# Kernel tuning notes

Hardware: AMD Instinct MI355X
Metric: run time of the kernel (lower is better)

## Reference

```python
import jax, jax.numpy as jnp
import numpy as np

EPS = 1e-12

def _spectral_normalize(W, u):
    # torch spectral_norm (eval-time math): v = normalize(W^T u), sigma = u^T W v
    u = jax.lax.stop_gradient(u)
    v = W.T @ u
    v = jax.lax.stop_gradient(v / (jnp.linalg.norm(v) + EPS))
    sigma = u @ (W @ v)
    return W / sigma

def _conv1x1(x, W):
    # 1x1 conv, no bias: (out,in) x (B,in,H,W) -> (B,out,H,W)
    return jnp.einsum('oc,bchw->bohw', W, x)

def setup_inputs() -> dict:
    key = jax.random.key(0)
    ks = jax.random.split(key, 10)
    B, C, H, W = 4, 512, 64, 64
    Cp = C // 8
    return {
        'x': jax.random.normal(ks[0], (B, C, H, W), jnp.float32),
        'Wf': jax.random.normal(ks[1], (Cp, C), jnp.float32) * 0.05,
        'Wg': jax.random.normal(ks[2], (Cp, C), jnp.float32) * 0.05,
        'Wh': jax.random.normal(ks[3], (Cp, C), jnp.float32) * 0.05,
        'Wv': jax.random.normal(ks[4], (C, Cp), jnp.float32) * 0.05,
        'uf': jax.random.normal(ks[5], (Cp,), jnp.float32),
        'ug': jax.random.normal(ks[6], (Cp,), jnp.float32),
        'uh': jax.random.normal(ks[7], (Cp,), jnp.float32),
        'uv': jax.random.normal(ks[8], (C,), jnp.float32),
        'gamma': jax.random.normal(ks[9], (1,), jnp.float32) * 0.1,
    }

def reference(x, Wf, Wg, Wh, Wv, uf, ug, uh, uv, gamma):
    B, C, H, W = x.shape
    Cp = Wf.shape[0]
    N = H * W
    Wf_sn = _spectral_normalize(Wf, uf)
    Wg_sn = _spectral_normalize(Wg, ug)
    Wh_sn = _spectral_normalize(Wh, uh)
    Wv_sn = _spectral_normalize(Wv, uv)
    fx = _conv1x1(x, Wf_sn).reshape(B, Cp, N)   # (B,Cp,N)
    gx = _conv1x1(x, Wg_sn).reshape(B, Cp, N)   # (B,Cp,N)
    # fx^T gx: (B,N,N), unscaled single-head attention, softmax over last dim
    scores = jnp.einsum('bcn,bcm->bnm', fx, gx)
    attn = jax.nn.softmax(scores, axis=-1)
    hx = _conv1x1(x, Wh_sn).reshape(B, Cp, N)
    # hx @ attn: out[b,c,j] = sum_i hx[b,c,i] * attn[b,i,j]
    out = jnp.einsum('bci,bij->bcj', hx, attn).reshape(B, Cp, H, W)
    unscaled = _conv1x1(out, Wv_sn)
    return gamma * unscaled + x
```

## Files before the change

### kernel.cpp

```cpp
#include <hip/hip_runtime.h>


#define NB 4
#define CC 512
#define CP 64
#define NN 4096
#define L2E 1.4426950408889634f

typedef __attribute__((ext_vector_type(8))) short short8;
typedef __attribute__((ext_vector_type(4))) float floatx4;
typedef __attribute__((ext_vector_type(16))) float floatx16;

#define MFMA32(A, B, C) __builtin_amdgcn_mfma_f32_32x32x16_bf16((A), (B), (C), 0, 0, 0)

__device__ __forceinline__ float bf2f_u(unsigned short h) {
    return __uint_as_float((unsigned)h << 16);
}
__device__ __forceinline__ float bf16lo(unsigned v) { return __uint_as_float(v << 16); }
__device__ __forceinline__ float bf16hi(unsigned v) { return __uint_as_float(v & 0xffff0000u); }
__device__ __forceinline__ unsigned short f2bf(float f) {
    unsigned u = __float_as_uint(f);
    u += 0x7fffu + ((u >> 16) & 1u);
    return (unsigned short)(u >> 16);
}
__device__ __forceinline__ unsigned pack2bf(float a, float b) {
    return (unsigned)f2bf(a) | ((unsigned)f2bf(b) << 16);
}
__device__ __forceinline__ float ldS(const void* p, long i, int f32) {
    return f32 ? ((const float*)p)[i] : bf2f_u(((const unsigned short*)p)[i]);
}
__device__ __forceinline__ float4 ld4(const void* p, long i, int f32) {
    if (f32) return *reinterpret_cast<const float4*>((const float*)p + i);
    uint2 v = *reinterpret_cast<const uint2*>((const unsigned short*)p + i);
    return make_float4(bf16lo(v.x), bf16hi(v.x), bf16lo(v.y), bf16hi(v.y));
}
__device__ __forceinline__ short8 frag8(const void* p, long i, int f32) {
    uint4 au;
    if (f32) {
        float4 v0 = *reinterpret_cast<const float4*>((const float*)p + i);
        float4 v1 = *reinterpret_cast<const float4*>((const float*)p + i + 4);
        au.x = pack2bf(v0.x, v0.y); au.y = pack2bf(v0.z, v0.w);
        au.z = pack2bf(v1.x, v1.y); au.w = pack2bf(v1.z, v1.w);
    } else {
        au = *reinterpret_cast<const uint4*>((const unsigned short*)p + i);
    }
    return *reinterpret_cast<short8*>(&au);
}
__device__ __forceinline__ short8 as_s8(uint4 v) { return *reinterpret_cast<short8*>(&v); }
__device__ __forceinline__ floatx16 zero16() {
    floatx16 z;
    #pragma unroll
    for (int i = 0; i < 16; ++i) z[i] = 0.f;
    return z;
}
__device__ __forceinline__ unsigned cvtpk_bf16(float a, float b) {
    unsigned r;
    asm("v_cvt_pk_bf16_f32 %0, %1, %2" : "=v"(r) : "v"(a), "v"(b));
    return r;
}
__device__ __forceinline__ void pl32swap(unsigned &a, unsigned &b) {
    asm("v_permlane32_swap_b32 %0, %1" : "+v"(a), "+v"(b));
}
__device__ __forceinline__ float rcpf(float x) {
    float r;
    asm("v_rcp_f32 %0, %1" : "=v"(r) : "v"(x));
    return r;
}
__device__ __forceinline__ float exp2a(float x) {
    float r;
    asm("v_exp_f32 %0, %1" : "=v"(r) : "v"(x));
    return r;
}

__global__ __launch_bounds__(256) void detect_kernel(
    const unsigned* __restrict__ x, int* __restrict__ flag)
{
    __shared__ int red[256];
    const int t = threadIdx.x;
    int bad = 0;
    for (int i = t; i < 4096; i += 256) {
        unsigned w = x[i];
        float f0 = __uint_as_float(w << 16);
        float f1 = __uint_as_float(w & 0xffff0000u);
        float a0 = fabsf(f0), a1 = fabsf(f1);
        if (!(a0 <= 1e3f) || (f0 != 0.f && a0 < 1e-20f)) bad++;
        if (!(a1 <= 1e3f) || (f1 != 0.f && a1 < 1e-20f)) bad++;
    }
    red[t] = bad;
    __syncthreads();
    for (int s = 128; s > 0; s >>= 1) { if (t < s) red[t] += red[t + s]; __syncthreads(); }
    if (t == 0) *flag = (red[0] > 64) ? 1 : 0;
}

__global__ __launch_bounds__(256) void xpose_kernel(
    const void* __restrict__ x, const int* __restrict__ dflag,
    unsigned short* __restrict__ xTF)
{
    const int f32 = *dflag;
    const int nt = blockIdx.x;
    const int b  = blockIdx.y;
    const int n0 = nt * 32;
    const int t = threadIdx.x;
    __shared__ unsigned short xl[32][72];

    const int n_l = t & 31, cg8 = ((t >> 5) & 7) * 8;
    const int q = t >> 6, lo = t & 63;

    for (int slab = 0; slab < 8; ++slab) {
        const int cs = slab * 64;
        float v[8];
        #pragma unroll
        for (int j = 0; j < 8; ++j)
            v[j] = ldS(x, ((long)b * CC + cs + cg8 + j) * NN + n0 + n_l, f32);
        if (slab) __syncthreads();
        unsigned* row = reinterpret_cast<unsigned*>(&xl[n_l][cg8]);
        row[0] = pack2bf(v[0], v[1]);
        row[1] = pack2bf(v[2], v[3]);
        row[2] = pack2bf(v[4], v[5]);
        row[3] = pack2bf(v[6], v[7]);
        __syncthreads();
        const int cb = q * 16 + ((lo >> 5) << 3);
        uint4 val = *reinterpret_cast<const uint4*>(&xl[lo & 31][cb]);
        size_t off = (((size_t)(b * 128 + nt) * 32) + slab * 4 + q) * 512 + (size_t)lo * 8;
        *reinterpret_cast<uint4*>(xTF + off) = val;
    }
}

__global__ __launch_bounds__(512) void sigma_kernel(
    const void* __restrict__ Wf, const void* __restrict__ Wg,
    const void* __restrict__ Wh, const void* __restrict__ Wv,
    const void* __restrict__ uf, const void* __restrict__ ug,
    const void* __restrict__ uh, const void* __restrict__ uv,
    const int* __restrict__ dflag, float* __restrict__ sig)
{
    const int f32 = *dflag;
    const int w = blockIdx.x;
    const void* W;
    const void* u;
    if (w == 0)      { W = Wf; u = uf; }
    else if (w == 1) { W = Wg; u = ug; }
    else if (w == 2) { W = Wh; u = uh; }
    else             { W = Wv; u = uv; }

    __shared__ float us[512];
    __shared__ float red[512];
    const int t = threadIdx.x;
    float S;

    if (w < 3) {
        if (t < 64) us[t] = ldS(u, t, f32);
        __syncthreads();
        float a = 0.f;
        #pragma unroll
        for (int i = 0; i < 64; ++i)
            a = fmaf(ldS(W, (long)i * 512 + t, f32), us[i], a);
        red[t] = a * a;
        __syncthreads();
        #pragma unroll
        for (int s = 256; s > 0; s >>= 1) {
            if (t < s) red[t] += red[t + s];
            __syncthreads();
        }
        S = red[0];
    } else {
        us[t] = ldS(u, t, f32);
        __syncthreads();
        const int g = t >> 6, c = t & 63;
        float a = 0.f;
        #pragma unroll
        for (int k = 0; k < 64; ++k) {
            int i = g + k * 8;
            a = fmaf(ldS(W, (long)i * 64 + c, f32), us[i], a);
        }
        red[t] = a;
        __syncthreads();
        #pragma unroll
        for (int s = 256; s >= 64; s >>= 1) {
            if (t < s) red[t] += red[t + s];
            __syncthreads();
        }
        float ac = (t < 64) ? red[t] : 0.f;
        __syncthreads();
        red[t] = ac * ac;
        __syncthreads();
        #pragma unroll
        for (int s = 256; s > 0; s >>= 1) {
            if (t < s) red[t] += red[t + s];
            __syncthreads();
        }
        S = red[0];
    }
    if (t == 0) sig[w] = (sqrtf(S) + 1e-12f) / S;
}

__global__ __launch_bounds__(256) void wprep_kernel(
    const void* __restrict__ Wf, const void* __restrict__ Wg,
    const void* __restrict__ Wh,
    const int* __restrict__ dflag, const float* __restrict__ sig,
    unsigned short* __restrict__ WF)
{
    const int f32 = *dflag;
    const int idx = blockIdx.x * 256 + threadIdx.x;
    const int l   = idx & 63;
    const int kc  = (idx >> 6) & 31;
    const int cpt = (idx >> 11) & 1;
    const int wi  = idx >> 12;
    const void* W = (wi == 0) ? Wf : ((wi == 1) ? Wg : Wh);
    const float sc = sig[wi] * (wi == 0 ? L2E : 1.f);
    const int cp = cpt * 32 + (l & 31);
    const int c  = kc * 16 + ((l >> 5) << 3);
    const long base = (long)cp * CC + c;
    float a0 = ldS(W, base + 0, f32) * sc, a1 = ldS(W, base + 1, f32) * sc;
    float a2 = ldS(W, base + 2, f32) * sc, a3 = ldS(W, base + 3, f32) * sc;
    float a4 = ldS(W, base + 4, f32) * sc, a5 = ldS(W, base + 5, f32) * sc;
    float a6 = ldS(W, base + 6, f32) * sc, a7 = ldS(W, base + 7, f32) * sc;
    uint4 o;
    o.x = pack2bf(a0, a1); o.y = pack2bf(a2, a3);
    o.z = pack2bf(a4, a5); o.w = pack2bf(a6, a7);
    *reinterpret_cast<uint4*>(WF + (size_t)idx * 8) = o;
}

__global__ __launch_bounds__(256, 4) void proj_kernel(
    const unsigned short* __restrict__ xTF,
    const unsigned short* __restrict__ WF,
    unsigned short* __restrict__ fxF, unsigned short* __restrict__ gxF,
    unsigned short* __restrict__ hxF)
{
    const int t = threadIdx.x;
    const int w = t >> 6, l = t & 63;
    const int b  = blockIdx.y;
    const int zc = blockIdx.z;
    const int wi = zc >> 1, cpt = zc & 1;
    const int nt = blockIdx.x * 4 + w;

    const unsigned short* xb = xTF + ((size_t)(b * 128 + nt) * 32) * 512 + (size_t)l * 8;
    const unsigned short* wb = WF + ((size_t)zc * 32) * 512 + (size_t)l * 8;

    floatx16 accE = zero16(), accO = zero16();
    uint4 x0 = *reinterpret_cast<const uint4*>(xb);
    uint4 w0 = *reinterpret_cast<const uint4*>(wb);
    uint4 x1, w1;

    if (wi == 2) {
        for (int kc = 0; kc < 32; kc += 2) {
            x1 = *reinterpret_cast<const uint4*>(xb + (kc + 1) * 512);
            w1 = *reinterpret_cast<const uint4*>(wb + (kc + 1) * 512);
            accE = MFMA32(as_s8(x0), as_s8(w0), accE);
            if (kc + 2 < 32) {
                x0 = *reinterpret_cast<const uint4*>(xb + (kc + 2) * 512);
                w0 = *reinterpret_cast<const uint4*>(wb + (kc + 2) * 512);
            }
            accO = MFMA32(as_s8(x1), as_s8(w1), accO);
        }
    } else {
        for (int kc = 0; kc < 32; kc += 2) {
            x1 = *reinterpret_cast<const uint4*>(xb + (kc + 1) * 512);
            w1 = *reinterpret_cast<const uint4*>(wb + (kc + 1) * 512);
            accE = MFMA32(as_s8(w0), as_s8(x0), accE);
            if (kc + 2 < 32) {
                x0 = *reinterpret_cast<const uint4*>(xb + (kc + 2) * 512);
                w0 = *reinterpret_cast<const uint4*>(wb + (kc + 2) * 512);
            }
            accO = MFMA32(as_s8(w1), as_s8(x1), accO);
        }
    }

    float a[16];
    #pragma unroll
    for (int i = 0; i < 16; ++i) a[i] = accE[i] + accO[i];

    if (wi < 2) {
        unsigned short* __restrict__ dstF = (wi == 0) ? fxF : gxF;
        #pragma unroll
        for (int kcl = 0; kcl < 2; ++kcl) {
            const int r8 = kcl * 8;
            unsigned u0 = cvtpk_bf16(a[r8 + 0], a[r8 + 1]);
            unsigned u1 = cvtpk_bf16(a[r8 + 2], a[r8 + 3]);
            unsigned u2 = cvtpk_bf16(a[r8 + 4], a[r8 + 5]);
            unsigned u3 = cvtpk_bf16(a[r8 + 6], a[r8 + 7]);
            pl32swap(u0, u2);
            pl32swap(u1, u3);
            uint4 o = make_uint4(u0, u1, u2, u3);
            size_t off = (((size_t)(b * 128 + nt) * 4) + cpt * 2 + kcl) * 512 + (size_t)l * 8;
            *reinterpret_cast<uint4*>(dstF + off) = o;
        }
    } else {
        #pragma unroll
        for (int ich = 0; ich < 2; ++ich) {
            const int r8 = ich * 8;
            unsigned u0 = cvtpk_bf16(a[r8 + 0], a[r8 + 1]);
            unsigned u1 = cvtpk_bf16(a[r8 + 2], a[r8 + 3]);
            unsigned u2 = cvtpk_bf16(a[r8 + 4], a[r8 + 5]);
            unsigned u3 = cvtpk_bf16(a[r8 + 6], a[r8 + 7]);
            pl32swap(u0, u2);
            pl32swap(u1, u3);
            uint4 o = make_uint4(u0, u1, u2, u3);
            size_t off = ((((size_t)(b * 128 + nt) * 2 + ich) * 2) + cpt) * 512 + (size_t)l * 8;
            *reinterpret_cast<uint4*>(hxF + off) = o;
        }
    }
}

__global__ __launch_bounds__(256, 4) void rowstats_kernel(
    const unsigned short* __restrict__ fxF, const unsigned short* __restrict__ gxF,
    float* __restrict__ rl)
{
    const int t = threadIdx.x;
    const int w = t >> 6, l = t & 63, l31 = l & 31, hi = l >> 5;
    const int b = blockIdx.z;
    const int i0 = blockIdx.x * 128 + w * 32;
    const int jbase = blockIdx.y * (NN / 8);

    __shared__ unsigned short stg[2][2048];

    const unsigned short* fA = fxF + ((size_t)(b * 128 + (i0 >> 5))) * 2048 + (size_t)l * 8;
    uint4 af[4];
    #pragma unroll
    for (int kc = 0; kc < 4; ++kc)
        af[kc] = *reinterpret_cast<const uint4*>(fA + kc * 512);

    const unsigned short* gB = gxF + ((size_t)(b * 128 + (jbase >> 5))) * 2048
                               + (size_t)w * 512 + (size_t)l * 8;

    float suml[16];
    #pragma unroll
    for (int r = 0; r < 16; ++r) suml[r] = 0.f;

    uint4 rg = *reinterpret_cast<const uint4*>(gB);
    *reinterpret_cast<uint4*>(&stg[0][w * 512 + l * 8]) = rg;
    __syncthreads();

    #pragma unroll 2
    for (int jt = 0; jt < 16; ++jt) {
        const int cur = jt & 1;
        if (jt + 1 < 16)
            rg = *reinterpret_cast<const uint4*>(gB + (size_t)(jt + 1) * 2048);

        uint4 bf[4];
        #pragma unroll
        for (int kc = 0; kc < 4; ++kc)
            bf[kc] = *reinterpret_cast<const uint4*>(&stg[cur][kc * 512 + l * 8]);

        floatx16 s = zero16();
        #pragma unroll
        for (int kc = 0; kc < 4; ++kc)
            s = MFMA32(as_s8(af[kc]), as_s8(bf[kc]), s);
        #pragma unroll
        for (int r = 0; r < 16; ++r) suml[r] += exp2a(s[r]);

        if (jt + 1 < 16)
            *reinterpret_cast<uint4*>(&stg[cur ^ 1][w * 512 + l * 8]) = rg;
        __syncthreads();
    }

    #pragma unroll
    for (int r = 0; r < 16; ++r) {
        float v = suml[r];
        v += __shfl_xor(v, 1);
        v += __shfl_xor(v, 2);
        v += __shfl_xor(v, 4);
        v += __shfl_xor(v, 8);
        v += __shfl_xor(v, 16);
        suml[r] = v;
    }
    if (l31 == 0) {
        #pragma unroll
        for (int r = 0; r < 16; ++r) {
            int row = (r & 3) + 8 * (r >> 2) + 4 * hi;
            atomicAdd(&rl[(size_t)b * NN + i0 + row], suml[r]);
        }
    }
}

__global__ __launch_bounds__(256) void scalehx_kernel(
    const float* __restrict__ rl, unsigned short* __restrict__ hxF)
{
    const int idx = blockIdx.x * 256 + threadIdx.x;
    const int l = idx & 63;
    const int r = idx >> 6;
    const int ich = (r >> 1) & 1;
    const int tile = (r >> 2) & 127;
    const int b = r >> 9;
    const int i0 = tile * 32 + ich * 16 + (l >> 5) * 8;
    const float* rp = rl + (size_t)b * NN + i0;
    float4 ra = *reinterpret_cast<const float4*>(rp);
    float4 rb = *reinterpret_cast<const float4*>(rp + 4);
    uint4 v = *reinterpret_cast<uint4*>(hxF + (size_t)idx * 8);
    uint4 ov;
    ov.x = pack2bf(bf16lo(v.x) * rcpf(ra.x), bf16hi(v.x) * rcpf(ra.y));
    ov.y = pack2bf(bf16lo(v.y) * rcpf(ra.z), bf16hi(v.y) * rcpf(ra.w));
    ov.z = pack2bf(bf16lo(v.z) * rcpf(rb.x), bf16hi(v.z) * rcpf(rb.y));
    ov.w = pack2bf(bf16lo(v.w) * rcpf(rb.z), bf16hi(v.w) * rcpf(rb.w));
    *reinterpret_cast<uint4*>(hxF + (size_t)idx * 8) = ov;
}

__global__ __launch_bounds__(256, 4) void pv_kernel(
    const unsigned short* __restrict__ fxF, const unsigned short* __restrict__ gxF,
    const unsigned short* __restrict__ hxF,
    float* __restrict__ opF0, float* __restrict__ opF1,
    float* __restrict__ opF2, float* __restrict__ opF3)
{
    const int t = threadIdx.x;
    const int w = t >> 6, l = t & 63, l31 = l & 31, hi = l >> 5;
    const int igrp = w >> 1, jgrp = w & 1;
    const int b = blockIdx.z;
    const int j0 = blockIdx.x * 64;
    const int isb = blockIdx.y;
    const int tbase = isb * 32 + igrp * 16;

    __shared__ unsigned short stg[2][2][2][2048];
    float* red = reinterpret_cast<float*>(stg);

    uint4 qf[4];
    {
        const unsigned short* gq =
            gxF + ((size_t)(b * 128 + (j0 >> 5) + jgrp)) * 2048 + (size_t)l * 8;
        #pragma unroll
        for (int kc = 0; kc < 4; ++kc)
            qf[kc] = *reinterpret_cast<const uint4*>(gq + kc * 512);
    }

    floatx16 acc0 = zero16(), acc1 = zero16();

    const unsigned short* sb =
        (jgrp == 0 ? fxF : hxF) + ((size_t)(b * 128 + tbase)) * 2048 + (size_t)l * 8;

    uint4 rg0 = *reinterpret_cast<const uint4*>(sb);
    uint4 rg1 = *reinterpret_cast<const uint4*>(sb + 512);
    uint4 rg2 = *reinterpret_cast<const uint4*>(sb + 1024);
    uint4 rg3 = *reinterpret_cast<const uint4*>(sb + 1536);
    {
        unsigned short* d = &stg[igrp][0][jgrp][l * 8];
        *reinterpret_cast<uint4*>(d)        = rg0;
        *reinterpret_cast<uint4*>(d + 512)  = rg1;
        *reinterpret_cast<uint4*>(d + 1024) = rg2;
        *reinterpret_cast<uint4*>(d + 1536) = rg3;
    }
    __syncthreads();

    #pragma unroll 2
    for (int it = 0; it < 16; ++it) {
        const int cur = it & 1;
        if (it + 1 < 16) {
            const unsigned short* p = sb + (size_t)(it + 1) * 2048;
            rg0 = *reinterpret_cast<const uint4*>(p);
            rg1 = *reinterpret_cast<const uint4*>(p + 512);
            rg2 = *reinterpret_cast<const uint4*>(p + 1024);
            rg3 = *reinterpret_cast<const uint4*>(p + 1536);
        }

        const unsigned short* fl = &stg[igrp][cur][0][l * 8];
        const unsigned short* vl = &stg[igrp][cur][1][l * 8];
        uint4 af[4], vf[4];
        #pragma unroll
        for (int kc = 0; kc < 4; ++kc)
            af[kc] = *reinterpret_cast<const uint4*>(fl + kc * 512);
        vf[0] = *reinterpret_cast<const uint4*>(vl);
        vf[1] = *reinterpret_cast<const uint4*>(vl + 1024);
        vf[2] = *reinterpret_cast<const uint4*>(vl + 512);
        vf[3] = *reinterpret_cast<const uint4*>(vl + 1536);

        floatx16 s = zero16();
        #pragma unroll
        for (int kc = 0; kc < 4; ++kc)
            s = MFMA32(as_s8(af[kc]), as_s8(qf[kc]), s);

        float e[16];
        #pragma unroll
        for (int r = 0; r < 16; ++r) e[r] = exp2a(s[r]);

        unsigned u0 = cvtpk_bf16(e[0], e[1]);
        unsigned u1 = cvtpk_bf16(e[2], e[3]);
        unsigned u2 = cvtpk_bf16(e[4], e[5]);
        unsigned u3 = cvtpk_bf16(e[6], e[7]);
        pl32swap(u0, u2);
        pl32swap(u1, u3);
        uint4 pa0 = make_uint4(u0, u1, u2, u3);
        unsigned u4 = cvtpk_bf16(e[8], e[9]);
        unsigned u5 = cvtpk_bf16(e[10], e[11]);
        unsigned u6 = cvtpk_bf16(e[12], e[13]);
        unsigned u7 = cvtpk_bf16(e[14], e[15]);
        pl32swap(u4, u6);
        pl32swap(u5, u7);
        uint4 pa1 = make_uint4(u4, u5, u6, u7);

        acc0 = MFMA32(as_s8(pa0), as_s8(vf[0]), acc0);
        acc0 = MFMA32(as_s8(pa1), as_s8(vf[1]), acc0);
        acc1 = MFMA32(as_s8(pa0), as_s8(vf[2]), acc1);
        acc1 = MFMA32(as_s8(pa1), as_s8(vf[3]), acc1);

        if (it + 1 < 16) {
            unsigned short* d = &stg[igrp][cur ^ 1][jgrp][l * 8];
            *reinterpret_cast<uint4*>(d)        = rg0;
            *reinterpret_cast<uint4*>(d + 512)  = rg1;
            *reinterpret_cast<uint4*>(d + 1024) = rg2;
            *reinterpret_cast<uint4*>(d + 1536) = rg3;
        }
        __syncthreads();
    }

    #pragma unroll
    for (int q = 0; q < 4; ++q)
        *reinterpret_cast<float4*>(&red[(q * 256 + t) * 4]) =
            make_float4(0.f, 0.f, 0.f, 0.f);
    __syncthreads();
    #pragma unroll
    for (int r = 0; r < 16; ++r) {
        int row = jgrp * 32 + (r & 3) + 8 * (r >> 2) + 4 * hi;
        atomicAdd(&red[row * 64 + l31],      acc0[r]);
        atomicAdd(&red[row * 64 + 32 + l31], acc1[r]);
    }
    __syncthreads();

    float* __restrict__ dst = (isb == 0) ? opF0 : ((isb == 1) ? opF1 : ((isb == 2) ? opF2 : opF3));
    #pragma unroll
    for (int q = 0; q < 4; ++q) {
        int idx = q * 256 + t;
        int e2  = idx & 1;
        int ll  = (idx >> 1) & 63;
        int ks  = (idx >> 7) & 1;
        int ntl = idx >> 8;
        int jloc = ntl * 16 + (ll & 15);
        int cp   = ks * 32 + ((ll >> 4) << 3) + e2 * 4;
        float4 v = *reinterpret_cast<const float4*>(&red[jloc * 64 + cp]);
        size_t off = (((size_t)(b * 256 + (j0 >> 4) + ntl) * 2 + ks) * 64 + ll) * 8 + e2 * 4;
        *reinterpret_cast<float4*>(dst + off) = v;
    }
}

__global__ __launch_bounds__(256) void outproj_kernel(
    const void* __restrict__ x,
    const void* __restrict__ Wv,
    const void* __restrict__ gamma,
    const int* __restrict__ dflag,
    const float* __restrict__ sig,
    const float* __restrict__ opF0, const float* __restrict__ opF1,
    const float* __restrict__ opF2, const float* __restrict__ opF3,
    void* __restrict__ y)
{
    const int f32 = *dflag;
    const int n0     = blockIdx.x * 64;
    const int cobase = blockIdx.y * 128;
    const int b      = blockIdx.z;
    const int t = threadIdx.x;
    const int wv = t >> 6, l = t & 63, l15 = l & 15, quad = l >> 4;
    const float scale = ldS(gamma, 0, f32) * sig[3];

    floatx4 acc[4][2];
    #pragma unroll
    for (int ns = 0; ns < 4; ++ns)
        #pragma unroll
        for (int ct = 0; ct < 2; ++ct) acc[ns][ct] = (floatx4){0.f, 0.f, 0.f, 0.f};

    #pragma unroll
    for (int ks = 0; ks < 2; ++ks) {
        short8 a[4];
        #pragma unroll
        for (int ns = 0; ns < 4; ++ns) {
            size_t fo = (((size_t)(b * 256 + (n0 >> 4) + ns) * 2 + ks) * 64 + l) * 8;
            float4 s0 = *reinterpret_cast<const float4*>(opF0 + fo);
            float4 s1 = *reinterpret_cast<const float4*>(opF1 + fo);
            float4 s2 = *reinterpret_cast<const float4*>(opF2 + fo);
            float4 s3 = *reinterpret_cast<const float4*>(opF3 + fo);
            float4 t0 = *reinterpret_cast<const float4*>(opF0 + fo + 4);
            float4 t1 = *reinterpret_cast<const float4*>(opF1 + fo + 4);
            float4 t2 = *reinterpret_cast<const float4*>(opF2 + fo + 4);
            float4 t3 = *reinterpret_cast<const float4*>(opF3 + fo + 4);
            float v0 = s0.x + s1.x + s2.x + s3.x;
            float v1 = s0.y + s1.y + s2.y + s3.y;
            float v2 = s0.z + s1.z + s2.z + s3.z;
            float v3 = s0.w + s1.w + s2.w + s3.w;
            float v4 = t0.x + t1.x + t2.x + t3.x;
            float v5 = t0.y + t1.y + t2.y + t3.y;
            float v6 = t0.z + t1.z + t2.z + t3.z;
            float v7 = t0.w + t1.w + t2.w + t3.w;
            uint4 au;
            au.x = pack2bf(v0, v1); au.y = pack2bf(v2, v3);
            au.z = pack2bf(v4, v5); au.w = pack2bf(v6, v7);
            a[ns] = *reinterpret_cast<short8*>(&au);
        }
        const int kb = ks * 32 + quad * 8;
        #pragma unroll
        for (int ct = 0; ct < 2; ++ct) {
            const int co = cobase + 32 * wv + 16 * ct + l15;
            short8 bfr = frag8(Wv, (long)co * CP + kb, f32);
            #pragma unroll
            for (int ns = 0; ns < 4; ++ns)
                acc[ns][ct] = __builtin_amdgcn_mfma_f32_16x16x32_bf16(
                    a[ns], bfr, acc[ns][ct], 0, 0, 0);
        }
    }

    #pragma unroll
    for (int ns = 0; ns < 4; ++ns)
        #pragma unroll
        for (int ct = 0; ct < 2; ++ct) {
            const int co = cobase + 32 * wv + 16 * ct + l15;
            const long base = ((long)b * CC + co) * NN + n0 + 16 * ns + quad * 4;
            float4 xv = ld4(x, base, f32);
            float o0 = fmaf(scale, acc[ns][ct][0], xv.x);
            float o1 = fmaf(scale, acc[ns][ct][1], xv.y);
            float o2 = fmaf(scale, acc[ns][ct][2], xv.z);
            float o3 = fmaf(scale, acc[ns][ct][3], xv.w);
            if (f32) {
                *reinterpret_cast<float4*>((float*)y + base) = make_float4(o0, o1, o2, o3);
            } else {
                uint2 o;
                o.x = pack2bf(o0, o1);
                o.y = pack2bf(o2, o3);
                *reinterpret_cast<uint2*>((unsigned short*)y + base) = o;
            }
        }
}

extern "C" void kernel_launch(void* const* d_in, const int* in_sizes, int n_in,
                              void* d_out, int out_size, void* d_ws, size_t ws_size,
                              hipStream_t stream)
{
    const void* x  = d_in[0];
    const void* Wf = d_in[1];
    const void* Wg = d_in[2];
    const void* Wh = d_in[3];
    const void* Wv = d_in[4];
    const void* uf = d_in[5];
    const void* ug = d_in[6];
    const void* uh = d_in[7];
    const void* uv = d_in[8];
    const void* gm = d_in[9];

    char* base = (char*)d_ws;
    int*   dfl = (int*)(base);
    float* sig = (float*)(base + 512);
    float* rl  = (float*)(base + 1024);
    float* opF0 = (float*)(base + 1024 + 65536);
    float* opF1 = opF0 + (size_t)NB * NN * CP;
    float* opF2 = opF1 + (size_t)NB * NN * CP;
    float* opF3 = opF2 + (size_t)NB * NN * CP;
    unsigned short* fxF = (unsigned short*)(opF3 + (size_t)NB * NN * CP);
    unsigned short* gxF = fxF + (size_t)NB * CP * NN;
    unsigned short* hxF = gxF + (size_t)NB * CP * NN;
    unsigned short* xTF = hxF + (size_t)NB * CP * NN;
    unsigned short* WF  = xTF + (size_t)NB * CC * NN;

    hipMemsetAsync(rl, 0, (size_t)NB * NN * sizeof(float), stream);

    hipLaunchKernelGGL(detect_kernel, dim3(1), dim3(256), 0, stream,
                       (const unsigned*)x, dfl);
    hipLaunchKernelGGL(xpose_kernel, dim3(128, NB), dim3(256), 0, stream,
                       x, dfl, xTF);
    hipLaunchKernelGGL(sigma_kernel, dim3(4), dim3(512), 0, stream,
                       Wf, Wg, Wh, Wv, uf, ug, uh, uv, dfl, sig);
    hipLaunchKernelGGL(wprep_kernel, dim3(48), dim3(256), 0, stream,
                       Wf, Wg, Wh, dfl, sig, WF);
    hipLaunchKernelGGL(proj_kernel, dim3(32, NB, 6), dim3(256), 0, stream,
                       xTF, WF, fxF, gxF, hxF);
    hipLaunchKernelGGL(rowstats_kernel, dim3(NN / 128, 8, NB), dim3(256), 0, stream,
                       fxF, gxF, rl);
    hipLaunchKernelGGL(scalehx_kernel, dim3((NB * CP * NN / 8) / 256), dim3(256), 0, stream,
                       rl, hxF);
    hipLaunchKernelGGL(pv_kernel, dim3(NN / 64, 4, NB), dim3(256), 0, stream,
                       fxF, gxF, hxF, opF0, opF1, opF2, opF3);
    hipLaunchKernelGGL(outproj_kernel, dim3(NN / 64, CC / 128, NB), dim3(256), 0, stream,
                       x, Wv, gm, dfl, sig, opF0, opF1, opF2, opF3, d_out);
}
```

Measured before the change: 226.4 us.

## Fuse memset and wprep into other kernels, remap grids for XCD locality

```diff
diff --git a/kernel.cpp b/kernel.cpp
--- a/kernel.cpp
+++ b/kernel.cpp
@@ -94,7 +94,7 @@
 
 __global__ __launch_bounds__(256) void xpose_kernel(
     const void* __restrict__ x, const int* __restrict__ dflag,
-    unsigned short* __restrict__ xTF)
+    unsigned short* __restrict__ xTF, float* __restrict__ rl)
 {
     const int f32 = *dflag;
     const int nt = blockIdx.x;
@@ -102,6 +102,9 @@
     const int n0 = nt * 32;
     const int t = threadIdx.x;
     __shared__ unsigned short xl[32][72];
+
+    const int gid = (b * 128 + nt) * 256 + t;
+    if (gid < NB * NN) rl[gid] = 0.f;
 
     const int n_l = t & 31, cg8 = ((t >> 5) & 7) * 8;
     const int q = t >> 6, lo = t & 63;
@@ -131,7 +134,8 @@
     const void* __restrict__ Wh, const void* __restrict__ Wv,
     const void* __restrict__ uf, const void* __restrict__ ug,
     const void* __restrict__ uh, const void* __restrict__ uv,
-    const int* __restrict__ dflag, float* __restrict__ sig)
+    const int* __restrict__ dflag, float* __restrict__ sig,
+    unsigned short* __restrict__ WF)
 {
     const int f32 = *dflag;
     const int w = blockIdx.x;
@@ -190,34 +194,30 @@
         }
         S = red[0];
     }
-    if (t == 0) sig[w] = (sqrtf(S) + 1e-12f) / S;
-}
-
-__global__ __launch_bounds__(256) void wprep_kernel(
-    const void* __restrict__ Wf, const void* __restrict__ Wg,
-    const void* __restrict__ Wh,
-    const int* __restrict__ dflag, const float* __restrict__ sig,
-    unsigned short* __restrict__ WF)
-{
-    const int f32 = *dflag;
-    const int idx = blockIdx.x * 256 + threadIdx.x;
-    const int l   = idx & 63;
-    const int kc  = (idx >> 6) & 31;
-    const int cpt = (idx >> 11) & 1;
-    const int wi  = idx >> 12;
-    const void* W = (wi == 0) ? Wf : ((wi == 1) ? Wg : Wh);
-    const float sc = sig[wi] * (wi == 0 ? L2E : 1.f);
-    const int cp = cpt * 32 + (l & 31);
-    const int c  = kc * 16 + ((l >> 5) << 3);
-    const long base = (long)cp * CC + c;
-    float a0 = ldS(W, base + 0, f32) * sc, a1 = ldS(W, base + 1, f32) * sc;
-    float a2 = ldS(W, base + 2, f32) * sc, a3 = ldS(W, base + 3, f32) * sc;
-    float a4 = ldS(W, base + 4, f32) * sc, a5 = ldS(W, base + 5, f32) * sc;
-    float a6 = ldS(W, base + 6, f32) * sc, a7 = ldS(W, base + 7, f32) * sc;
-    uint4 o;
-    o.x = pack2bf(a0, a1); o.y = pack2bf(a2, a3);
-    o.z = pack2bf(a4, a5); o.w = pack2bf(a6, a7);
-    *reinterpret_cast<uint4*>(WF + (size_t)idx * 8) = o;
+    const float isig = (sqrtf(S) + 1e-12f) / S;
+    if (t == 0) sig[w] = isig;
+
+    if (w < 3) {
+        const float sc = isig * (w == 0 ? L2E : 1.f);
+        #pragma unroll
+        for (int q = 0; q < 8; ++q) {
+            const int idx = q * 512 + t;
+            const int ll  = idx & 63;
+            const int kc  = (idx >> 6) & 31;
+            const int cpt = idx >> 11;
+            const int cp = cpt * 32 + (ll & 31);
+            const int c  = kc * 16 + ((ll >> 5) << 3);
+            const long base = (long)cp * CC + c;
+            float a0 = ldS(W, base + 0, f32) * sc, a1 = ldS(W, base + 1, f32) * sc;
+            float a2 = ldS(W, base + 2, f32) * sc, a3 = ldS(W, base + 3, f32) * sc;
+            float a4 = ldS(W, base + 4, f32) * sc, a5 = ldS(W, base + 5, f32) * sc;
+            float a6 = ldS(W, base + 6, f32) * sc, a7 = ldS(W, base + 7, f32) * sc;
+            uint4 o;
+            o.x = pack2bf(a0, a1); o.y = pack2bf(a2, a3);
+            o.z = pack2bf(a4, a5); o.w = pack2bf(a6, a7);
+            *reinterpret_cast<uint4*>(WF + ((size_t)w * 4096 + idx) * 8) = o;
+        }
+    }
 }
 
 __global__ __launch_bounds__(256, 4) void proj_kernel(
@@ -228,10 +228,14 @@
 {
     const int t = threadIdx.x;
     const int w = t >> 6, l = t & 63;
-    const int b  = blockIdx.y;
-    const int zc = blockIdx.z;
-    const int wi = zc >> 1, cpt = zc & 1;
-    const int nt = blockIdx.x * 4 + w;
+    const int flat = blockIdx.x;
+    const int k = flat & 7, s = flat >> 3;
+    const int sd6 = s / 6;
+    const int g = (k << 4) + sd6;
+    const int zc = s - sd6 * 6;
+    const int b = g & 3;
+    const int nt = (g >> 2) * 4 + w;
+    const int wi = zc >> 1;
 
     const unsigned short* xb = xTF + ((size_t)(b * 128 + nt) * 32) * 512 + (size_t)l * 8;
     const unsigned short* wb = WF + ((size_t)zc * 32) * 512 + (size_t)l * 8;
@@ -269,6 +273,7 @@
     #pragma unroll
     for (int i = 0; i < 16; ++i) a[i] = accE[i] + accO[i];
 
+    const int cpt = zc & 1;
     if (wi < 2) {
         unsigned short* __restrict__ dstF = (wi == 0) ? fxF : gxF;
         #pragma unroll
@@ -307,11 +312,15 @@
 {
     const int t = threadIdx.x;
     const int w = t >> 6, l = t & 63, l31 = l & 31, hi = l >> 5;
-    const int b = blockIdx.z;
-    const int i0 = blockIdx.x * 128 + w * 32;
-    const int jbase = blockIdx.y * (NN / 8);
-
-    __shared__ unsigned short stg[2][2048];
+    const int flat = blockIdx.x;
+    const int k = flat & 7, s = flat >> 3;
+    const int c2 = (k << 2) + (s >> 5);
+    const int iblk = s & 31;
+    const int jy = c2 & 7, b = c2 >> 3;
+    const int i0 = iblk * 128 + w * 32;
+    const int jbase = jy * 512;
+
+    __shared__ unsigned short stg[2][2][2048];
 
     const unsigned short* fA = fxF + ((size_t)(b * 128 + (i0 >> 5))) * 2048 + (size_t)l * 8;
     uint4 af[4];
@@ -326,30 +335,40 @@
     #pragma unroll
     for (int r = 0; r < 16; ++r) suml[r] = 0.f;
 
-    uint4 rg = *reinterpret_cast<const uint4*>(gB);
-    *reinterpret_cast<uint4*>(&stg[0][w * 512 + l * 8]) = rg;
+    uint4 ra = *reinterpret_cast<const uint4*>(gB);
+    uint4 rb = *reinterpret_cast<const uint4*>(gB + 2048);
+    *reinterpret_cast<uint4*>(&stg[0][0][w * 512 + l * 8]) = ra;
+    *reinterpret_cast<uint4*>(&stg[0][1][w * 512 + l * 8]) = rb;
     __syncthreads();
 
     #pragma unroll 2
-    for (int jt = 0; jt < 16; ++jt) {
-        const int cur = jt & 1;
-        if (jt + 1 < 16)
-            rg = *reinterpret_cast<const uint4*>(gB + (size_t)(jt + 1) * 2048);
-
-        uint4 bf[4];
-        #pragma unroll
-        for (int kc = 0; kc < 4; ++kc)
-            bf[kc] = *reinterpret_cast<const uint4*>(&stg[cur][kc * 512 + l * 8]);
-
-        floatx16 s = zero16();
-        #pragma unroll
-        for (int kc = 0; kc < 4; ++kc)
-            s = MFMA32(as_s8(af[kc]), as_s8(bf[kc]), s);
-        #pragma unroll
-        for (int r = 0; r < 16; ++r) suml[r] += exp2a(s[r]);
-
-        if (jt + 1 < 16)
-            *reinterpret_cast<uint4*>(&stg[cur ^ 1][w * 512 + l * 8]) = rg;
+    for (int p = 0; p < 8; ++p) {
+        const int cur = p & 1;
+        if (p + 1 < 8) {
+            ra = *reinterpret_cast<const uint4*>(gB + (size_t)(2 * p + 2) * 2048);
+            rb = *reinterpret_cast<const uint4*>(gB + (size_t)(2 * p + 3) * 2048);
+        }
+
+        uint4 bfA[4], bfB[4];
+        #pragma unroll
+        for (int kc = 0; kc < 4; ++kc) {
+            bfA[kc] = *reinterpret_cast<const uint4*>(&stg[cur][0][kc * 512 + l * 8]);
+            bfB[kc] = *reinterpret_cast<const uint4*>(&stg[cur][1][kc * 512 + l * 8]);
+        }
+
+        floatx16 sA = zero16(), sB = zero16();
+        #pragma unroll
+        for (int kc = 0; kc < 4; ++kc) {
+            sA = MFMA32(as_s8(af[kc]), as_s8(bfA[kc]), sA);
+            sB = MFMA32(as_s8(af[kc]), as_s8(bfB[kc]), sB);
+        }
+        #pragma unroll
+        for (int r = 0; r < 16; ++r) suml[r] += exp2a(sA[r]) + exp2a(sB[r]);
+
+        if (p + 1 < 8) {
+            *reinterpret_cast<uint4*>(&stg[cur ^ 1][0][w * 512 + l * 8]) = ra;
+            *reinterpret_cast<uint4*>(&stg[cur ^ 1][1][w * 512 + l * 8]) = rb;
+        }
         __syncthreads();
     }
 
@@ -403,9 +422,12 @@
     const int t = threadIdx.x;
     const int w = t >> 6, l = t & 63, l31 = l & 31, hi = l >> 5;
     const int igrp = w >> 1, jgrp = w & 1;
-    const int b = blockIdx.z;
-    const int j0 = blockIdx.x * 64;
-    const int isb = blockIdx.y;
+    const int flat = blockIdx.x;
+    const int k = flat & 7, s = flat >> 3;
+    const int c2 = (k << 1) + (s >> 6);
+    const int jblk = s & 63;
+    const int isb = c2 & 3, b = c2 >> 2;
+    const int j0 = jblk * 64;
     const int tbase = isb * 32 + igrp * 16;
 
     __shared__ unsigned short stg[2][2][2][2048];
@@ -460,14 +482,14 @@
         vf[2] = *reinterpret_cast<const uint4*>(vl + 512);
         vf[3] = *reinterpret_cast<const uint4*>(vl + 1536);
 
-        floatx16 s = zero16();
+        floatx16 s2 = zero16();
         #pragma unroll
         for (int kc = 0; kc < 4; ++kc)
-            s = MFMA32(as_s8(af[kc]), as_s8(qf[kc]), s);
+            s2 = MFMA32(as_s8(af[kc]), as_s8(qf[kc]), s2);
 
         float e[16];
         #pragma unroll
-        for (int r = 0; r < 16; ++r) e[r] = exp2a(s[r]);
+        for (int r = 0; r < 16; ++r) e[r] = exp2a(s2[r]);
 
         unsigned u0 = cvtpk_bf16(e[0], e[1]);
         unsigned u1 = cvtpk_bf16(e[2], e[3]);
@@ -642,23 +664,19 @@
     unsigned short* xTF = hxF + (size_t)NB * CP * NN;
     unsigned short* WF  = xTF + (size_t)NB * CC * NN;
 
-    hipMemsetAsync(rl, 0, (size_t)NB * NN * sizeof(float), stream);
-
     hipLaunchKernelGGL(detect_kernel, dim3(1), dim3(256), 0, stream,
                        (const unsigned*)x, dfl);
     hipLaunchKernelGGL(xpose_kernel, dim3(128, NB), dim3(256), 0, stream,
-                       x, dfl, xTF);
+                       x, dfl, xTF, rl);
     hipLaunchKernelGGL(sigma_kernel, dim3(4), dim3(512), 0, stream,
-                       Wf, Wg, Wh, Wv, uf, ug, uh, uv, dfl, sig);
-    hipLaunchKernelGGL(wprep_kernel, dim3(48), dim3(256), 0, stream,
-                       Wf, Wg, Wh, dfl, sig, WF);
-    hipLaunchKernelGGL(proj_kernel, dim3(32, NB, 6), dim3(256), 0, stream,
+                       Wf, Wg, Wh, Wv, uf, ug, uh, uv, dfl, sig, WF);
+    hipLaunchKernelGGL(proj_kernel, dim3(768), dim3(256), 0, stream,
                        xTF, WF, fxF, gxF, hxF);
-    hipLaunchKernelGGL(rowstats_kernel, dim3(NN / 128, 8, NB), dim3(256), 0, stream,
+    hipLaunchKernelGGL(rowstats_kernel, dim3(1024), dim3(256), 0, stream,
                        fxF, gxF, rl);
     hipLaunchKernelGGL(scalehx_kernel, dim3((NB * CP * NN / 8) / 256), dim3(256), 0, stream,
                        rl, hxF);
-    hipLaunchKernelGGL(pv_kernel, dim3(NN / 64, 4, NB), dim3(256), 0, stream,
+    hipLaunchKernelGGL(pv_kernel, dim3(1024), dim3(256), 0, stream,
                        fxF, gxF, hxF, opF0, opF1, opF2, opF3);
     hipLaunchKernelGGL(outproj_kernel, dim3(NN / 64, CC / 128, NB), dim3(256), 0, stream,
                        x, Wv, gm, dfl, sig, opF0, opF1, opF2, opF3, d_out);
```

Result: slower. 238.2 us (+5.2%).
